# Performance work log

Hardware: AMD Instinct MI355X
Metric: run time of the kernel (lower is better)

The kernel has to match this reference:

```python
import jax, jax.numpy as jnp
import numpy as np

EPS = 1e-6

def setup_inputs() -> dict:
    key = jax.random.key(0)
    ks = jax.random.split(key, 8)
    D = 64
    x = jax.random.normal(ks[0], (32, 56, 56, 4 * D), jnp.float32)
    beta = jnp.zeros((1, 1, 1, 4 * D), jnp.float32)
    diag = lambda k: 0.5 + 0.1 * jax.random.uniform(k, (D,), jnp.float32)
    off = lambda k: 0.05 * jax.random.normal(k, (D,), jnp.float32)
    k2 = jax.random.split(ks[1], 10)
    return dict(
        x=x, beta=beta,
        gam_rr=diag(k2[0]), gam_ri=off(k2[1]), gam_rj=off(k2[2]), gam_rk=off(k2[3]),
        gam_ii=diag(k2[4]), gam_ij=off(k2[5]), gam_ik=off(k2[6]),
        gam_jj=diag(k2[7]), gam_jk=off(k2[8]), gam_kk=diag(k2[9]),
    )

def _hbn(x, beta, gam_rr, gam_ri, gam_rj, gam_rk, gam_ii, gam_ij, gam_ik, gam_jj, gam_jk, gam_kk):
    # Training-mode quaternion/tessarine whitening BN (activation_position='after').
    N, H, W, C = x.shape
    d = C // 4
    mean = jnp.mean(x, axis=(0, 1, 2))           # [C]
    c = x - mean
    r, i, j, k = jnp.split(c, 4, axis=-1)        # each [N,H,W,d]
    m = lambda a, b: jnp.mean(a * b, axis=(0, 1, 2))  # [d]
    Vrr = m(r, r) + EPS; Vri = m(r, i); Vrj = m(r, j); Vrk = m(r, k)
    Vii = m(i, i) + EPS; Vij = m(i, j); Vik = m(i, k)
    Vjj = m(j, j) + EPS; Vjk = m(j, k); Vkk = m(k, k) + EPS
    # Symmetric 4x4 covariance per channel -> [d,4,4]
    V = jnp.stack([
        jnp.stack([Vrr, Vri, Vrj, Vrk], -1),
        jnp.stack([Vri, Vii, Vij, Vik], -1),
        jnp.stack([Vrj, Vij, Vjj, Vjk], -1),
        jnp.stack([Vrk, Vik, Vjk, Vkk], -1)], -2)
    # Whitening matrix W = V^{-1/2} (ZCA) via symmetric eigendecomposition
    w, U = jnp.linalg.eigh(V)
    Wm = jnp.einsum('dab,db,dcb->dac', U, 1.0 / jnp.sqrt(w), U)  # [d,4,4]
    v = jnp.stack([r, i, j, k], axis=-1)         # [N,H,W,d,4]
    xh = jnp.einsum('dec,nhwdc->nhwde', Wm, v)   # whitened components
    # 10-parameter symmetric affine recombination
    G = jnp.stack([
        jnp.stack([gam_rr, gam_ri, gam_rj, gam_rk], -1),
        jnp.stack([gam_ri, gam_ii, gam_ij, gam_ik], -1),
        jnp.stack([gam_rj, gam_ij, gam_jj, gam_jk], -1),
        jnp.stack([gam_rk, gam_ik, gam_jk, gam_kk], -1)], -2)  # [d,4,4]
    y = jnp.einsum('dec,nhwdc->nhwde', G, xh)
    y = jnp.concatenate([y[..., 0], y[..., 1], y[..., 2], y[..., 3]], axis=-1) + beta
    return jax.nn.elu(y)

def reference(x, beta, gam_rr, gam_ri, gam_rj, gam_rk, gam_ii, gam_ij, gam_ik, gam_jj, gam_jk, gam_kk):
    return _hbn(x, beta, gam_rr, gam_ri, gam_rj, gam_rk, gam_ii, gam_ij, gam_ik, gam_jj, gam_jk, gam_kk)
```

## Files before the change

### kernel.cpp

```cpp
#include <hip/hip_runtime.h>
#include <math.h>

static constexpr int NPOS = 32 * 56 * 56;
static constexpr int CCH  = 256;
static constexpr int RB   = 512;
static constexpr int ABLK = 2048;
static constexpr double EPSV = 1e-6;

typedef float f32x4 __attribute__((ext_vector_type(4)));


__device__ __forceinline__ float eluf(float v) {
  return v > 0.f ? v : (__expf(v) - 1.f);
}

__global__ __launch_bounds__(256) void hbn_reduce(const float* __restrict__ x,
                                                  float* __restrict__ partial) {
  const int tid  = threadIdx.x;
  const int lane = tid & 63;
  const int wib  = tid >> 6;
  const int dq   = lane & 15;
  const int gw   = blockIdx.x * 4 + wib;
  const int nw   = RB * 4;

  __shared__ float stage[4][256];
  __shared__ float outs[4][896];
  float* st = &stage[wib][0];

  float acc[14][4];
#pragma unroll
  for (int s = 0; s < 14; ++s)
#pragma unroll
    for (int t = 0; t < 4; ++t) acc[s][t] = 0.f;

  for (int p = gw; p < NPOS; p += nw) {
    const f32x4 v = *reinterpret_cast<const f32x4*>(x + (size_t)p * CCH + lane * 4);
    *reinterpret_cast<f32x4*>(st + lane * 4) = v;
    const f32x4 r4 = *reinterpret_cast<const f32x4*>(st + 0   + dq * 4);
    const f32x4 i4 = *reinterpret_cast<const f32x4*>(st + 64  + dq * 4);
    const f32x4 j4 = *reinterpret_cast<const f32x4*>(st + 128 + dq * 4);
    const f32x4 k4 = *reinterpret_cast<const f32x4*>(st + 192 + dq * 4);
#pragma unroll
    for (int t = 0; t < 4; ++t) {
      const float r = r4[t], i = i4[t], j = j4[t], k = k4[t];
      acc[0][t] += r;  acc[1][t] += i;  acc[2][t] += j;  acc[3][t] += k;
      acc[4][t]  = fmaf(r, r, acc[4][t]);
      acc[5][t]  = fmaf(r, i, acc[5][t]);
      acc[6][t]  = fmaf(r, j, acc[6][t]);
      acc[7][t]  = fmaf(r, k, acc[7][t]);
      acc[8][t]  = fmaf(i, i, acc[8][t]);
      acc[9][t]  = fmaf(i, j, acc[9][t]);
      acc[10][t] = fmaf(i, k, acc[10][t]);
      acc[11][t] = fmaf(j, j, acc[11][t]);
      acc[12][t] = fmaf(j, k, acc[12][t]);
      acc[13][t] = fmaf(k, k, acc[13][t]);
    }
  }

  if (lane < 16) {
#pragma unroll
    for (int s = 0; s < 14; ++s)
#pragma unroll
      for (int t = 0; t < 4; ++t)
        outs[wib][s * 64 + dq * 4 + t] = acc[s][t];
  }
  __syncthreads();
  float* dst = partial + (size_t)blockIdx.x * 896;
  for (int idx = tid; idx < 896; idx += 256)
    dst[idx] = outs[0][idx] + outs[1][idx] + outs[2][idx] + outs[3][idx];
}

__global__ __launch_bounds__(64) void hbn_sum(const float* __restrict__ partial,
                                              double* __restrict__ S) {
  const int s = blockIdx.x;
  const int t = threadIdx.x;
  double a = 0.0;
#pragma unroll
  for (int k = 0; k < RB / 64; ++k)
    a += (double)partial[(size_t)(k * 64 + t) * 896 + s];
#pragma unroll
  for (int off = 32; off; off >>= 1) a += __shfl_down(a, off);
  if (t == 0) S[s] = a;
}

__global__ void hbn_solve(const double* __restrict__ S,
                          const float* __restrict__ beta,
                          const float* __restrict__ grr, const float* __restrict__ gri,
                          const float* __restrict__ grj, const float* __restrict__ grk,
                          const float* __restrict__ gii, const float* __restrict__ gij,
                          const float* __restrict__ gik, const float* __restrict__ gjj,
                          const float* __restrict__ gjk, const float* __restrict__ gkk,
                          float* __restrict__ Mt, float* __restrict__ offv) {
  const int d = threadIdx.x;
  const double invM = 1.0 / (double)NPOS;

  double mu[4];
  mu[0] = S[0*64+d]*invM; mu[1] = S[1*64+d]*invM;
  mu[2] = S[2*64+d]*invM; mu[3] = S[3*64+d]*invM;

  float A[4][4];
  A[0][0] = (float)(S[4*64+d]*invM  - mu[0]*mu[0] + EPSV);
  A[0][1] = A[1][0] = (float)(S[5*64+d]*invM  - mu[0]*mu[1]);
  A[0][2] = A[2][0] = (float)(S[6*64+d]*invM  - mu[0]*mu[2]);
  A[0][3] = A[3][0] = (float)(S[7*64+d]*invM  - mu[0]*mu[3]);
  A[1][1] = (float)(S[8*64+d]*invM  - mu[1]*mu[1] + EPSV);
  A[1][2] = A[2][1] = (float)(S[9*64+d]*invM  - mu[1]*mu[2]);
  A[1][3] = A[3][1] = (float)(S[10*64+d]*invM - mu[1]*mu[3]);
  A[2][2] = (float)(S[11*64+d]*invM - mu[2]*mu[2] + EPSV);
  A[2][3] = A[3][2] = (float)(S[12*64+d]*invM - mu[2]*mu[3]);
  A[3][3] = (float)(S[13*64+d]*invM - mu[3]*mu[3] + EPSV);

  float U[4][4] = {{1,0,0,0},{0,1,0,0},{0,0,1,0},{0,0,0,1}};

#pragma unroll 1
  for (int sweep = 0; sweep < 6; ++sweep) {
#pragma unroll
    for (int p = 0; p < 3; ++p) {
#pragma unroll
      for (int q = p + 1; q < 4; ++q) {
        float apq = A[p][q];
        if (fabsf(apq) > 1e-30f) {
          float theta = (A[q][q] - A[p][p]) / (2.0f * apq);
          float t = 1.0f / (fabsf(theta) + sqrtf(fmaf(theta, theta, 1.0f)));
          if (theta < 0.0f) t = -t;
          float c = rsqrtf(fmaf(t, t, 1.0f));
          float s = t * c;
#pragma unroll
          for (int r = 0; r < 4; ++r) {
            float arp = A[r][p], arq = A[r][q];
            A[r][p] = c*arp - s*arq;  A[r][q] = s*arp + c*arq;
          }
#pragma unroll
          for (int r = 0; r < 4; ++r) {
            float apr = A[p][r], aqr = A[q][r];
            A[p][r] = c*apr - s*aqr;  A[q][r] = s*apr + c*aqr;
          }
#pragma unroll
          for (int r = 0; r < 4; ++r) {
            float urp = U[r][p], urq = U[r][q];
            U[r][p] = c*urp - s*urq;  U[r][q] = s*urp + c*urq;
          }
        }
      }
    }
  }

  float wis[4];
#pragma unroll
  for (int b = 0; b < 4; ++b) {
    float w = A[b][b];
    if (w < 1e-12f) w = 1e-12f;
    wis[b] = rsqrtf(w);
  }

  float Wm[4][4];
#pragma unroll
  for (int a = 0; a < 4; ++a)
#pragma unroll
    for (int cc = 0; cc < 4; ++cc) {
      float acc = 0.0f;
#pragma unroll
      for (int b = 0; b < 4; ++b) acc += U[a][b] * wis[b] * U[cc][b];
      Wm[a][cc] = acc;
    }

  float G[4][4];
  G[0][0] = grr[d]; G[0][1] = G[1][0] = gri[d];
  G[0][2] = G[2][0] = grj[d]; G[0][3] = G[3][0] = grk[d];
  G[1][1] = gii[d]; G[1][2] = G[2][1] = gij[d];
  G[1][3] = G[3][1] = gik[d];
  G[2][2] = gjj[d]; G[2][3] = G[3][2] = gjk[d];
  G[3][3] = gkk[d];

  float M[4][4];
#pragma unroll
  for (int e = 0; e < 4; ++e)
#pragma unroll
    for (int cc = 0; cc < 4; ++cc) {
      float acc = 0.0f;
#pragma unroll
      for (int b = 0; b < 4; ++b) acc += G[e][b] * Wm[b][cc];
      M[e][cc] = acc;
      Mt[(e*4 + cc)*64 + d] = acc;
    }

#pragma unroll
  for (int e = 0; e < 4; ++e) {
    float acc = beta[e*64 + d];
#pragma unroll
    for (int cc = 0; cc < 4; ++cc) acc -= M[e][cc] * (float)mu[cc];
    offv[e*64 + d] = acc;
  }
}

__global__ __launch_bounds__(256) void hbn_apply(const float* __restrict__ x,
                                                 const float* __restrict__ Mt,
                                                 const float* __restrict__ offv,
                                                 float* __restrict__ out) {
  const int tid  = threadIdx.x;
  const int lane = tid & 63;
  const int wib  = tid >> 6;
  const int dq   = lane & 15;
  const int e    = lane >> 4;
  const int gw   = blockIdx.x * 4 + wib;
  const int nw   = ABLK * 4;

  __shared__ float stage[4][256];
  float* st = &stage[wib][0];

  f32x4 me[4];
#pragma unroll
  for (int c = 0; c < 4; ++c)
    me[c] = *reinterpret_cast<const f32x4*>(Mt + (e*4 + c)*64 + dq*4);
  const f32x4 ob = *reinterpret_cast<const f32x4*>(offv + e*64 + dq*4);

  for (int p = gw; p < NPOS; p += nw) {
    const f32x4 v = *reinterpret_cast<const f32x4*>(x + (size_t)p * CCH + lane * 4);
    *reinterpret_cast<f32x4*>(st + lane * 4) = v;
    const f32x4 r4 = *reinterpret_cast<const f32x4*>(st + 0   + dq * 4);
    const f32x4 i4 = *reinterpret_cast<const f32x4*>(st + 64  + dq * 4);
    const f32x4 j4 = *reinterpret_cast<const f32x4*>(st + 128 + dq * 4);
    const f32x4 k4 = *reinterpret_cast<const f32x4*>(st + 192 + dq * 4);

    f32x4 y;
#pragma unroll
    for (int t = 0; t < 4; ++t)
      y[t] = fmaf(me[0][t], r4[t],
             fmaf(me[1][t], i4[t],
             fmaf(me[2][t], j4[t],
             fmaf(me[3][t], k4[t], ob[t]))));
#pragma unroll
    for (int t = 0; t < 4; ++t) y[t] = eluf(y[t]);
    __builtin_nontemporal_store(y, reinterpret_cast<f32x4*>(out + (size_t)p * CCH + lane * 4));
  }
}

extern "C" void kernel_launch(void* const* d_in, const int* in_sizes, int n_in,
                              void* d_out, int out_size, void* d_ws, size_t ws_size,
                              hipStream_t stream) {
  (void)in_sizes; (void)n_in; (void)out_size; (void)ws_size;
  const float* x    = (const float*)d_in[0];
  const float* beta = (const float*)d_in[1];
  const float* grr  = (const float*)d_in[2];
  const float* gri  = (const float*)d_in[3];
  const float* grj  = (const float*)d_in[4];
  const float* grk  = (const float*)d_in[5];
  const float* gii  = (const float*)d_in[6];
  const float* gij  = (const float*)d_in[7];
  const float* gik  = (const float*)d_in[8];
  const float* gjj  = (const float*)d_in[9];
  const float* gjk  = (const float*)d_in[10];
  const float* gkk  = (const float*)d_in[11];
  float* out = (float*)d_out;

  double* S      = (double*)d_ws;
  float*  Mt     = (float*)((char*)d_ws + 7168);
  float*  offv   = (float*)((char*)d_ws + 11264);
  float*  partial= (float*)((char*)d_ws + 12288);

  hbn_reduce<<<RB, 256, 0, stream>>>(x, partial);
  hbn_sum<<<896, 64, 0, stream>>>(partial, S);
  hbn_solve<<<1, 64, 0, stream>>>(S, beta, grr, gri, grj, grk,
                                  gii, gij, gik, gjj, gjk, gkk, Mt, offv);
  hbn_apply<<<ABLK, 256, 0, stream>>>(x, Mt, offv, out);
}
```

Before: 75.99 us.

## Fuse solve into apply, double reduce grid with 2-position unroll, pack sum blocks

The separate single-block solve kernel is removed. Every apply block now recomputes the per-channel eigen-whitening and affine matrices redundantly in its first wave and keeps them in shared memory, which drops one launch and its serialization gap. The reduce kernel doubles its block count and processes two positions per iteration to raise memory-level parallelism. The sum kernel packs four reductions per 256-thread block. The cost is redundant eigensolves in each of the 2048 apply blocks and a larger partial buffer for the sum kernel to read.

```diff
diff --git a/kernel.cpp b/kernel.cpp
--- a/kernel.cpp
+++ b/kernel.cpp
@@ -3,7 +3,7 @@
 
 static constexpr int NPOS = 32 * 56 * 56;
 static constexpr int CCH  = 256;
-static constexpr int RB   = 512;
+static constexpr int RB   = 1024;
 static constexpr int ABLK = 2048;
 static constexpr double EPSV = 1e-6;
 
@@ -23,7 +23,7 @@
   const int gw   = blockIdx.x * 4 + wib;
   const int nw   = RB * 4;
 
-  __shared__ float stage[4][256];
+  __shared__ float stage[4][512];
   __shared__ float outs[4][896];
   float* st = &stage[wib][0];
 
@@ -33,27 +33,32 @@
 #pragma unroll
     for (int t = 0; t < 4; ++t) acc[s][t] = 0.f;
 
-  for (int p = gw; p < NPOS; p += nw) {
-    const f32x4 v = *reinterpret_cast<const f32x4*>(x + (size_t)p * CCH + lane * 4);
-    *reinterpret_cast<f32x4*>(st + lane * 4) = v;
-    const f32x4 r4 = *reinterpret_cast<const f32x4*>(st + 0   + dq * 4);
-    const f32x4 i4 = *reinterpret_cast<const f32x4*>(st + 64  + dq * 4);
-    const f32x4 j4 = *reinterpret_cast<const f32x4*>(st + 128 + dq * 4);
-    const f32x4 k4 = *reinterpret_cast<const f32x4*>(st + 192 + dq * 4);
-#pragma unroll
-    for (int t = 0; t < 4; ++t) {
-      const float r = r4[t], i = i4[t], j = j4[t], k = k4[t];
-      acc[0][t] += r;  acc[1][t] += i;  acc[2][t] += j;  acc[3][t] += k;
-      acc[4][t]  = fmaf(r, r, acc[4][t]);
-      acc[5][t]  = fmaf(r, i, acc[5][t]);
-      acc[6][t]  = fmaf(r, j, acc[6][t]);
-      acc[7][t]  = fmaf(r, k, acc[7][t]);
-      acc[8][t]  = fmaf(i, i, acc[8][t]);
-      acc[9][t]  = fmaf(i, j, acc[9][t]);
-      acc[10][t] = fmaf(i, k, acc[10][t]);
-      acc[11][t] = fmaf(j, j, acc[11][t]);
-      acc[12][t] = fmaf(j, k, acc[12][t]);
-      acc[13][t] = fmaf(k, k, acc[13][t]);
+  for (int p0 = gw * 2; p0 < NPOS; p0 += nw * 2) {
+    const f32x4 va = *reinterpret_cast<const f32x4*>(x + (size_t)p0 * CCH + lane * 4);
+    const f32x4 vb = *reinterpret_cast<const f32x4*>(x + (size_t)(p0 + 1) * CCH + lane * 4);
+    *reinterpret_cast<f32x4*>(st + lane * 4)       = va;
+    *reinterpret_cast<f32x4*>(st + 256 + lane * 4) = vb;
+#pragma unroll
+    for (int h = 0; h < 2; ++h) {
+      const f32x4 r4 = *reinterpret_cast<const f32x4*>(st + h*256 + 0   + dq * 4);
+      const f32x4 i4 = *reinterpret_cast<const f32x4*>(st + h*256 + 64  + dq * 4);
+      const f32x4 j4 = *reinterpret_cast<const f32x4*>(st + h*256 + 128 + dq * 4);
+      const f32x4 k4 = *reinterpret_cast<const f32x4*>(st + h*256 + 192 + dq * 4);
+#pragma unroll
+      for (int t = 0; t < 4; ++t) {
+        const float r = r4[t], i = i4[t], j = j4[t], k = k4[t];
+        acc[0][t] += r;  acc[1][t] += i;  acc[2][t] += j;  acc[3][t] += k;
+        acc[4][t]  = fmaf(r, r, acc[4][t]);
+        acc[5][t]  = fmaf(r, i, acc[5][t]);
+        acc[6][t]  = fmaf(r, j, acc[6][t]);
+        acc[7][t]  = fmaf(r, k, acc[7][t]);
+        acc[8][t]  = fmaf(i, i, acc[8][t]);
+        acc[9][t]  = fmaf(i, j, acc[9][t]);
+        acc[10][t] = fmaf(i, k, acc[10][t]);
+        acc[11][t] = fmaf(j, j, acc[11][t]);
+        acc[12][t] = fmaf(j, k, acc[12][t]);
+        acc[13][t] = fmaf(k, k, acc[13][t]);
+      }
     }
   }
 
@@ -70,30 +75,29 @@
     dst[idx] = outs[0][idx] + outs[1][idx] + outs[2][idx] + outs[3][idx];
 }
 
-__global__ __launch_bounds__(64) void hbn_sum(const float* __restrict__ partial,
-                                              double* __restrict__ S) {
-  const int s = blockIdx.x;
-  const int t = threadIdx.x;
+__global__ __launch_bounds__(256) void hbn_sum(const float* __restrict__ partial,
+                                               double* __restrict__ S) {
+  const int lane = threadIdx.x & 63;
+  const int s    = blockIdx.x * 4 + (threadIdx.x >> 6);
+  if (s >= 896) return;
   double a = 0.0;
 #pragma unroll
   for (int k = 0; k < RB / 64; ++k)
-    a += (double)partial[(size_t)(k * 64 + t) * 896 + s];
+    a += (double)partial[(size_t)(k * 64 + lane) * 896 + s];
 #pragma unroll
   for (int off = 32; off; off >>= 1) a += __shfl_down(a, off);
-  if (t == 0) S[s] = a;
-}
-
-__global__ void hbn_solve(const double* __restrict__ S,
-                          const float* __restrict__ beta,
-                          const float* __restrict__ grr, const float* __restrict__ gri,
-                          const float* __restrict__ grj, const float* __restrict__ grk,
-                          const float* __restrict__ gii, const float* __restrict__ gij,
-                          const float* __restrict__ gik, const float* __restrict__ gjj,
-                          const float* __restrict__ gjk, const float* __restrict__ gkk,
-                          float* __restrict__ Mt, float* __restrict__ offv) {
-  const int d = threadIdx.x;
+  if (lane == 0) S[s] = a;
+}
+
+__device__ __forceinline__ void solve_one(const double* __restrict__ S,
+                                          const float* __restrict__ beta,
+                                          const float* __restrict__ grr, const float* __restrict__ gri,
+                                          const float* __restrict__ grj, const float* __restrict__ grk,
+                                          const float* __restrict__ gii, const float* __restrict__ gij,
+                                          const float* __restrict__ gik, const float* __restrict__ gjj,
+                                          const float* __restrict__ gjk, const float* __restrict__ gkk,
+                                          int d, float* Mout , float* offout ) {
   const double invM = 1.0 / (double)NPOS;
-
   double mu[4];
   mu[0] = S[0*64+d]*invM; mu[1] = S[1*64+d]*invM;
   mu[2] = S[2*64+d]*invM; mu[3] = S[3*64+d]*invM;
@@ -181,7 +185,7 @@
 #pragma unroll
       for (int b = 0; b < 4; ++b) acc += G[e][b] * Wm[b][cc];
       M[e][cc] = acc;
-      Mt[(e*4 + cc)*64 + d] = acc;
+      Mout[e*4 + cc] = acc;
     }
 
 #pragma unroll
@@ -189,13 +193,18 @@
     float acc = beta[e*64 + d];
 #pragma unroll
     for (int cc = 0; cc < 4; ++cc) acc -= M[e][cc] * (float)mu[cc];
-    offv[e*64 + d] = acc;
+    offout[e] = acc;
   }
 }
 
 __global__ __launch_bounds__(256) void hbn_apply(const float* __restrict__ x,
-                                                 const float* __restrict__ Mt,
-                                                 const float* __restrict__ offv,
+                                                 const double* __restrict__ S,
+                                                 const float* __restrict__ beta,
+                                                 const float* __restrict__ grr, const float* __restrict__ gri,
+                                                 const float* __restrict__ grj, const float* __restrict__ grk,
+                                                 const float* __restrict__ gii, const float* __restrict__ gij,
+                                                 const float* __restrict__ gik, const float* __restrict__ gjj,
+                                                 const float* __restrict__ gjk, const float* __restrict__ gkk,
                                                  float* __restrict__ out) {
   const int tid  = threadIdx.x;
   const int lane = tid & 63;
@@ -206,13 +215,26 @@
   const int nw   = ABLK * 4;
 
   __shared__ float stage[4][256];
+  __shared__ float Ms[64 * 16];
+  __shared__ float offs[256];
   float* st = &stage[wib][0];
 
+  if (tid < 64) {
+    float Mo[16], oo[4];
+    solve_one(S, beta, grr, gri, grj, grk, gii, gij, gik, gjj, gjk, gkk,
+              tid, Mo, oo);
+#pragma unroll
+    for (int ec = 0; ec < 16; ++ec) Ms[ec * 64 + tid] = Mo[ec];
+#pragma unroll
+    for (int q = 0; q < 4; ++q) offs[q * 64 + tid] = oo[q];
+  }
+  __syncthreads();
+
   f32x4 me[4];
 #pragma unroll
   for (int c = 0; c < 4; ++c)
-    me[c] = *reinterpret_cast<const f32x4*>(Mt + (e*4 + c)*64 + dq*4);
-  const f32x4 ob = *reinterpret_cast<const f32x4*>(offv + e*64 + dq*4);
+    me[c] = *reinterpret_cast<const f32x4*>(Ms + (e*4 + c)*64 + dq*4);
+  const f32x4 ob = *reinterpret_cast<const f32x4*>(offs + e*64 + dq*4);
 
   for (int p = gw; p < NPOS; p += nw) {
     const f32x4 v = *reinterpret_cast<const f32x4*>(x + (size_t)p * CCH + lane * 4);
@@ -254,13 +276,10 @@
   float* out = (float*)d_out;
 
   double* S      = (double*)d_ws;
-  float*  Mt     = (float*)((char*)d_ws + 7168);
-  float*  offv   = (float*)((char*)d_ws + 11264);
   float*  partial= (float*)((char*)d_ws + 12288);
 
   hbn_reduce<<<RB, 256, 0, stream>>>(x, partial);
-  hbn_sum<<<896, 64, 0, stream>>>(partial, S);
-  hbn_solve<<<1, 64, 0, stream>>>(S, beta, grr, gri, grj, grk,
-                                  gii, gij, gik, gjj, gjk, gkk, Mt, offv);
-  hbn_apply<<<ABLK, 256, 0, stream>>>(x, Mt, offv, out);
-}
+  hbn_sum<<<224, 256, 0, stream>>>(partial, S);
+  hbn_apply<<<ABLK, 256, 0, stream>>>(x, S, beta, grr, gri, grj, grk,
+                                      gii, gij, gik, gjj, gjk, gkk, out);
+}
```

After: 69.69 us. 1.09x faster.
